# Kernel optimization log

Measured on AMD Instinct MI355X. Metric: run time of the kernel, lower is better.

The kernel has to match this reference:

```python
import jax, jax.numpy as jnp
import numpy as np

LN_EPS = 1e-10


def _log_g(x):
    # log of g(x) where g(x) = x + 0.5 for x >= 0 else sigmoid(x)
    return jnp.where(x >= 0, jnp.log(jax.nn.relu(x) + 0.5), -jax.nn.softplus(-x))


def setup_inputs() -> dict:
    key = jax.random.key(0)
    k1, k2 = jax.random.split(key)
    B, T, D, H = 8, 4096, 512, 512
    x = jax.random.normal(k1, (B, T, D), dtype=jnp.float32)
    ln_gamma = jnp.ones((D,), dtype=jnp.float32)
    ln_beta = jnp.zeros((D,), dtype=jnp.float32)
    W_gh = jax.random.normal(k2, (D, 2 * H), dtype=jnp.float32) * 0.02
    return {"x": x, "ln_gamma": ln_gamma, "ln_beta": ln_beta, "W_gh": W_gh}


def reference(x, ln_gamma, ln_beta, W_gh):
    # LayerNorm over last dim
    mu = jnp.mean(x, axis=-1, keepdims=True)
    var = jnp.mean(jnp.square(x - mu), axis=-1, keepdims=True)
    xn = (x - mu) * jax.lax.rsqrt(var + LN_EPS) * ln_gamma + ln_beta

    # minGRU projection: gate logits k and candidate pre-activation
    gh = jnp.einsum('btd,dh->bth', xn, W_gh)  # [B, T, 2H]
    H = W_gh.shape[1] // 2
    k_gate, h_pre = gh[..., :H], gh[..., H:]

    # log-space parallel scan (Heinsen): h_t = (1-z_t) h_{t-1} + z_t g(h_pre_t)
    log_z = -jax.nn.softplus(-k_gate)        # log sigmoid(k)
    log_coeffs = -jax.nn.softplus(k_gate)    # log(1 - sigmoid(k))
    log_values = log_z + _log_g(h_pre)

    a_star = jnp.cumsum(log_coeffs, axis=1)
    log_h = a_star + jax.lax.cumlogsumexp(log_values - a_star, axis=1)
    h = jnp.exp(log_h)  # [B, T, H]

    # residual (res_proj is Identity since input_size == hidden_size)
    out = h + x
    hidden = h[:, -1]  # last hidden state [B, H]
    return out, hidden
```

## Files before the change

kernel.cpp:

```cpp
#include <hip/hip_runtime.h>
#include <stdint.h>

#define NB 8
#define NT 4096
#define ND 512
#define NH 512
#define NN 1024
#define NM (NB * NT)
#define NK 512
#define NCH 64
#define CTS 64

typedef __bf16 bf16x8 __attribute__((ext_vector_type(8)));
typedef float floatx4 __attribute__((ext_vector_type(4)));
typedef unsigned int uint_g __attribute__((address_space(1)));
typedef unsigned int uint_l __attribute__((address_space(3)));

__device__ __forceinline__ float bf2f(unsigned short u) {
    union { unsigned int i; float f; } v; v.i = ((unsigned int)u) << 16; return v.f;
}
__device__ __forceinline__ unsigned short f2bf(float f) {
    union { float f; unsigned int i; } v; v.f = f;
    return (unsigned short)((v.i + 0x7FFFu + ((v.i >> 16) & 1u)) >> 16);
}

__device__ __forceinline__ void load_lds16(const void* g, void* l) {
    __builtin_amdgcn_global_load_lds((const uint_g*)g, (uint_l*)l, 16, 0, 0);
}

__global__ __launch_bounds__(256) void ln_kernel(const float* __restrict__ x,
                                                 const float* __restrict__ gamma,
                                                 const float* __restrict__ beta,
                                                 unsigned short* __restrict__ xn) {
    int row = blockIdx.x;
    int tid = threadIdx.x;
    float2 v = ((const float2*)(x + (size_t)row * ND))[tid];
    float s  = v.x + v.y;
    float sq = v.x * v.x + v.y * v.y;
#pragma unroll
    for (int off = 32; off > 0; off >>= 1) {
        s  += __shfl_down(s,  off, 64);
        sq += __shfl_down(sq, off, 64);
    }
    __shared__ float ps[4], psq[4];
    __shared__ float smu, srstd;
    int wid = tid >> 6, lane = tid & 63;
    if (lane == 0) { ps[wid] = s; psq[wid] = sq; }
    __syncthreads();
    if (tid == 0) {
        float ts = ps[0] + ps[1] + ps[2] + ps[3];
        float tq = psq[0] + psq[1] + psq[2] + psq[3];
        float mu  = ts * (1.0f / ND);
        float var = tq * (1.0f / ND) - mu * mu;
        smu = mu; srstd = rsqrtf(var + 1e-10f);
    }
    __syncthreads();
    float mu = smu, rstd = srstd;
    float2 g = ((const float2*)gamma)[tid];
    float2 b = ((const float2*)beta)[tid];
    ushort2 o;
    o.x = f2bf((v.x - mu) * rstd * g.x + b.x);
    o.y = f2bf((v.y - mu) * rstd * g.y + b.y);
    ((ushort2*)(xn + (size_t)row * ND))[tid] = o;
}

__global__ __launch_bounds__(256) void wt_kernel(const float* __restrict__ W,
                                                 unsigned short* __restrict__ Wt) {
    __shared__ float tile[32][33];
    int n0 = blockIdx.x * 32;
    int k0 = blockIdx.y * 32;
    int tx = threadIdx.x, ty = threadIdx.y;
#pragma unroll
    for (int j = 0; j < 4; ++j)
        tile[ty + j * 8][tx] = W[(size_t)(k0 + ty + j * 8) * NN + n0 + tx];
    __syncthreads();
#pragma unroll
    for (int j = 0; j < 4; ++j)
        Wt[(size_t)(n0 + ty + j * 8) * NK + k0 + tx] = f2bf(tile[tx][ty + j * 8]);
}

__global__ __launch_bounds__(256) void gemm_kernel(const unsigned short* __restrict__ A,
                                                   const unsigned short* __restrict__ Bt,
                                                   unsigned short* __restrict__ C) {
    __shared__ __align__(16) unsigned short As[128 * 64];
    __shared__ __align__(16) unsigned short Bs[128 * 64];
    int tid  = threadIdx.x;
    int lane = tid & 63;
    int wid  = tid >> 6;
    int wm = wid & 1, wn = wid >> 1;
    int bx = blockIdx.x;
    int mt = bx & 255;
    int nt = bx >> 8;
    const int Rm = mt * 128, Rn = nt * 128;

    int rloc = lane >> 3;
    int cl   = lane & 7;
    int cg   = cl ^ rloc;

    int frow = lane & 15;
    int quad = lane >> 4;
    int fx   = lane & 7;

    floatx4 acc[4][4];
#pragma unroll
    for (int i = 0; i < 4; ++i)
#pragma unroll
        for (int j = 0; j < 4; ++j)
            acc[i][j] = (floatx4){0.f, 0.f, 0.f, 0.f};

#pragma unroll 1
    for (int kt = 0; kt < NK / 64; ++kt) {
        int k0 = kt * 64;
        __syncthreads();
#pragma unroll
        for (int s = 0; s < 4; ++s) {
            int g  = wid * 4 + s;
            int ml = g * 8 + rloc;
            load_lds16(A + (size_t)(Rm + ml) * NK + k0 + cg * 8, As + g * 512);
        }
#pragma unroll
        for (int s = 0; s < 4; ++s) {
            int g  = wid * 4 + s;
            int nl = g * 8 + rloc;
            load_lds16(Bt + (size_t)(Rn + nl) * NK + k0 + cg * 8, Bs + g * 512);
        }
        __syncthreads();
#pragma unroll
        for (int ks = 0; ks < 2; ++ks) {
            int ch = (ks * 4 + quad) ^ fx;
            bf16x8 af[4], bfr[4];
#pragma unroll
            for (int mi = 0; mi < 4; ++mi) {
                int ml = wm * 64 + mi * 16 + frow;
                af[mi] = *(const bf16x8*)(As + ml * 64 + ch * 8);
            }
#pragma unroll
            for (int ni = 0; ni < 4; ++ni) {
                int nl = wn * 64 + ni * 16 + frow;
                bfr[ni] = *(const bf16x8*)(Bs + nl * 64 + ch * 8);
            }
#pragma unroll
            for (int mi = 0; mi < 4; ++mi)
#pragma unroll
                for (int ni = 0; ni < 4; ++ni)
                    acc[mi][ni] = __builtin_amdgcn_mfma_f32_16x16x32_bf16(
                        af[mi], bfr[ni], acc[mi][ni], 0, 0, 0);
        }
    }
#pragma unroll
    for (int mi = 0; mi < 4; ++mi)
#pragma unroll
        for (int ni = 0; ni < 4; ++ni)
#pragma unroll
            for (int r = 0; r < 4; ++r) {
                int row = Rm + wm * 64 + mi * 16 + quad * 4 + r;
                int col = Rn + wn * 64 + ni * 16 + frow;
                C[(size_t)row * NN + col] = f2bf(acc[mi][ni][r]);
            }
}

__device__ __forceinline__ void gate_av(unsigned short ku, unsigned short pu,
                                        float& a, float& v) {
    float k = bf2f(ku), p = bf2f(pu);
    float e = __expf(k);
    a = 1.0f / (1.0f + e);
    float z = e * a;
    float g = (p >= 0.0f) ? (p + 0.5f) : 1.0f / (1.0f + __expf(-p));
    v = z * g;
}

__global__ __launch_bounds__(256) void scan1_kernel(const unsigned short* __restrict__ gh,
                                                    float* __restrict__ cA,
                                                    float* __restrict__ cV) {
    int blk = blockIdx.x;
    int b = blk >> 6, c = blk & 63;
    int h = threadIdx.x * 2;
    const unsigned short* base = gh + ((size_t)(b * NT + c * CTS)) * NN;
    float A0 = 1.f, V0 = 0.f, A1 = 1.f, V1 = 0.f;
#pragma unroll 4
    for (int t = 0; t < CTS; ++t) {
        const unsigned short* p = base + (size_t)t * NN;
        ushort2 kk = *(const ushort2*)(p + h);
        ushort2 hh = *(const ushort2*)(p + NH + h);
        float a0, v0, a1, v1;
        gate_av(kk.x, hh.x, a0, v0);
        gate_av(kk.y, hh.y, a1, v1);
        V0 = a0 * V0 + v0;  A0 *= a0;
        V1 = a1 * V1 + v1;  A1 *= a1;
    }
    size_t o = ((size_t)(b * NCH + c)) * NH + h;
    *(float2*)(cA + o) = make_float2(A0, A1);
    *(float2*)(cV + o) = make_float2(V0, V1);
}

__global__ __launch_bounds__(256) void scan2_kernel(const float* __restrict__ cA,
                                                    const float* __restrict__ cV,
                                                    float* __restrict__ hinit) {
    int w = (blockIdx.x * 256 + threadIdx.x) >> 6;
    int lane = threadIdx.x & 63;
    int b = w >> 9, h = w & 511;
    size_t o = ((size_t)(b * NCH + lane)) * NH + h;
    float A = cA[o], V = cV[o];
#pragma unroll
    for (int off = 1; off < 64; off <<= 1) {
        float Ap = __shfl_up(A, off, 64);
        float Vp = __shfl_up(V, off, 64);
        if (lane >= off) { V = A * Vp + V; A = A * Ap; }
    }
    float Vp = __shfl_up(V, 1, 64);
    hinit[o] = (lane == 0) ? 0.f : Vp;
}

__global__ __launch_bounds__(256) void scan3_kernel(const unsigned short* __restrict__ gh,
                                                    const float* __restrict__ hinit,
                                                    const float* __restrict__ x,
                                                    float* __restrict__ out,
                                                    float* __restrict__ hidden) {
    int blk = blockIdx.x;
    int b = blk >> 6, c = blk & 63;
    int h = threadIdx.x * 2;
    size_t row0 = (size_t)(b * NT + c * CTS);
    const unsigned short* base = gh + row0 * NN;
    const float* xb = x + row0 * ND;
    float* ob = out + row0 * ND;
    float2 hs = *(const float2*)(hinit + ((size_t)(b * NCH + c)) * NH + h);
    float h0 = hs.x, h1 = hs.y;
#pragma unroll 4
    for (int t = 0; t < CTS; ++t) {
        const unsigned short* p = base + (size_t)t * NN;
        ushort2 kk = *(const ushort2*)(p + h);
        ushort2 hh = *(const ushort2*)(p + NH + h);
        float a0, v0, a1, v1;
        gate_av(kk.x, hh.x, a0, v0);
        gate_av(kk.y, hh.y, a1, v1);
        h0 = a0 * h0 + v0;
        h1 = a1 * h1 + v1;
        float2 xv = *(const float2*)(xb + (size_t)t * ND + h);
        *(float2*)(ob + (size_t)t * ND + h) = make_float2(h0 + xv.x, h1 + xv.y);
    }
    if (c == NCH - 1)
        *(float2*)(hidden + (size_t)b * NH + h) = make_float2(h0, h1);
}

extern "C" void kernel_launch(void* const* d_in, const int* in_sizes, int n_in,
                              void* d_out, int out_size, void* d_ws, size_t ws_size,
                              hipStream_t stream) {
    const float* x     = (const float*)d_in[0];
    const float* gamma = (const float*)d_in[1];
    const float* beta  = (const float*)d_in[2];
    const float* W     = (const float*)d_in[3];

    float* out    = (float*)d_out;
    float* hidden = out + (size_t)NM * ND;

    char* ws = (char*)d_ws;
    unsigned short* Wt = (unsigned short*)ws;
    unsigned short* gh = (unsigned short*)(ws + (size_t)(1u << 20));
    float* cA    = (float*)(ws + (size_t)(1u << 20) + (size_t)NM * NN * 2);
    float* cV    = cA + (size_t)NB * NCH * NH;
    float* hinit = cV + (size_t)NB * NCH * NH;
    unsigned short* xn = (unsigned short*)d_out;

    wt_kernel<<<dim3(32, 16), dim3(32, 8), 0, stream>>>(W, Wt);
    ln_kernel<<<NM, 256, 0, stream>>>(x, gamma, beta, xn);
    gemm_kernel<<<2048, 256, 0, stream>>>(xn, Wt, gh);
    scan1_kernel<<<NB * NCH, 256, 0, stream>>>(gh, cA, cV);
    scan2_kernel<<<1024, 256, 0, stream>>>(cA, cV, hinit);
    scan3_kernel<<<NB * NCH, 256, 0, stream>>>(gh, hinit, x, out, hidden);
}
```

Baseline: 260.7 us.

## Rework layernorm per-wave, reorder GEMM tiles, and widen chunked scan kernels

New measurement: 231.8 us. -11.1%, faster.

```diff
diff --git a/kernel.cpp b/kernel.cpp
--- a/kernel.cpp
+++ b/kernel.cpp
@@ -8,8 +8,8 @@
 #define NN 1024
 #define NM (NB * NT)
 #define NK 512
-#define NCH 64
-#define CTS 64
+#define NCH 128
+#define CTS 32
 
 typedef __bf16 bf16x8 __attribute__((ext_vector_type(8)));
 typedef float floatx4 __attribute__((ext_vector_type(4)));
@@ -32,36 +32,38 @@
                                                  const float* __restrict__ gamma,
                                                  const float* __restrict__ beta,
                                                  unsigned short* __restrict__ xn) {
-    int row = blockIdx.x;
-    int tid = threadIdx.x;
-    float2 v = ((const float2*)(x + (size_t)row * ND))[tid];
-    float s  = v.x + v.y;
-    float sq = v.x * v.x + v.y * v.y;
+    int wid = threadIdx.x >> 6, lane = threadIdx.x & 63;
+    size_t row = (size_t)blockIdx.x * 4 + wid;
+    const float4* xr = (const float4*)(x + row * ND);
+    float4 v0 = xr[lane];
+    float4 v1 = xr[lane + 64];
+    float s  = (v0.x + v0.y) + (v0.z + v0.w) + (v1.x + v1.y) + (v1.z + v1.w);
+    float sq = v0.x * v0.x + v0.y * v0.y + v0.z * v0.z + v0.w * v0.w
+             + v1.x * v1.x + v1.y * v1.y + v1.z * v1.z + v1.w * v1.w;
 #pragma unroll
     for (int off = 32; off > 0; off >>= 1) {
-        s  += __shfl_down(s,  off, 64);
-        sq += __shfl_down(sq, off, 64);
-    }
-    __shared__ float ps[4], psq[4];
-    __shared__ float smu, srstd;
-    int wid = tid >> 6, lane = tid & 63;
-    if (lane == 0) { ps[wid] = s; psq[wid] = sq; }
-    __syncthreads();
-    if (tid == 0) {
-        float ts = ps[0] + ps[1] + ps[2] + ps[3];
-        float tq = psq[0] + psq[1] + psq[2] + psq[3];
-        float mu  = ts * (1.0f / ND);
-        float var = tq * (1.0f / ND) - mu * mu;
-        smu = mu; srstd = rsqrtf(var + 1e-10f);
-    }
-    __syncthreads();
-    float mu = smu, rstd = srstd;
-    float2 g = ((const float2*)gamma)[tid];
-    float2 b = ((const float2*)beta)[tid];
-    ushort2 o;
-    o.x = f2bf((v.x - mu) * rstd * g.x + b.x);
-    o.y = f2bf((v.y - mu) * rstd * g.y + b.y);
-    ((ushort2*)(xn + (size_t)row * ND))[tid] = o;
+        s  += __shfl_xor(s,  off, 64);
+        sq += __shfl_xor(sq, off, 64);
+    }
+    float mu   = s * (1.0f / ND);
+    float var  = sq * (1.0f / ND) - mu * mu;
+    float rstd = rsqrtf(var + 1e-10f);
+    const float4* gr = (const float4*)gamma;
+    const float4* br = (const float4*)beta;
+    float4 g0 = gr[lane], g1 = gr[lane + 64];
+    float4 b0 = br[lane], b1 = br[lane + 64];
+    ushort4 o0, o1;
+    o0.x = f2bf((v0.x - mu) * rstd * g0.x + b0.x);
+    o0.y = f2bf((v0.y - mu) * rstd * g0.y + b0.y);
+    o0.z = f2bf((v0.z - mu) * rstd * g0.z + b0.z);
+    o0.w = f2bf((v0.w - mu) * rstd * g0.w + b0.w);
+    o1.x = f2bf((v1.x - mu) * rstd * g1.x + b1.x);
+    o1.y = f2bf((v1.y - mu) * rstd * g1.y + b1.y);
+    o1.z = f2bf((v1.z - mu) * rstd * g1.z + b1.z);
+    o1.w = f2bf((v1.w - mu) * rstd * g1.w + b1.w);
+    ushort4* xo = (ushort4*)(xn + row * ND);
+    xo[lane]      = o0;
+    xo[lane + 64] = o1;
 }
 
 __global__ __launch_bounds__(256) void wt_kernel(const float* __restrict__ W,
@@ -89,8 +91,8 @@
     int wid  = tid >> 6;
     int wm = wid & 1, wn = wid >> 1;
     int bx = blockIdx.x;
-    int mt = bx & 255;
-    int nt = bx >> 8;
+    int nt = bx & 7;
+    int mt = bx >> 3;
     const int Rm = mt * 128, Rn = nt * 128;
 
     int rloc = lane >> 3;
@@ -163,83 +165,93 @@
                                         float& a, float& v) {
     float k = bf2f(ku), p = bf2f(pu);
     float e = __expf(k);
-    a = 1.0f / (1.0f + e);
+    a = __builtin_amdgcn_rcpf(1.0f + e);
     float z = e * a;
-    float g = (p >= 0.0f) ? (p + 0.5f) : 1.0f / (1.0f + __expf(-p));
+    float gneg = __builtin_amdgcn_rcpf(1.0f + __expf(-p));
+    float g = (p >= 0.0f) ? (p + 0.5f) : gneg;
     v = z * g;
 }
 
-__global__ __launch_bounds__(256) void scan1_kernel(const unsigned short* __restrict__ gh,
+__global__ __launch_bounds__(128) void scan1_kernel(const unsigned short* __restrict__ gh,
                                                     float* __restrict__ cA,
                                                     float* __restrict__ cV) {
-    int blk = blockIdx.x;
-    int b = blk >> 6, c = blk & 63;
-    int h = threadIdx.x * 2;
+    int b = blockIdx.x >> 7, c = blockIdx.x & 127;
+    int h = threadIdx.x * 4;
     const unsigned short* base = gh + ((size_t)(b * NT + c * CTS)) * NN;
-    float A0 = 1.f, V0 = 0.f, A1 = 1.f, V1 = 0.f;
-#pragma unroll 4
+    float A0 = 1.f, A1 = 1.f, A2 = 1.f, A3 = 1.f;
+    float V0 = 0.f, V1 = 0.f, V2 = 0.f, V3 = 0.f;
+#pragma unroll 8
     for (int t = 0; t < CTS; ++t) {
         const unsigned short* p = base + (size_t)t * NN;
-        ushort2 kk = *(const ushort2*)(p + h);
-        ushort2 hh = *(const ushort2*)(p + NH + h);
-        float a0, v0, a1, v1;
-        gate_av(kk.x, hh.x, a0, v0);
-        gate_av(kk.y, hh.y, a1, v1);
-        V0 = a0 * V0 + v0;  A0 *= a0;
-        V1 = a1 * V1 + v1;  A1 *= a1;
-    }
-    size_t o = ((size_t)(b * NCH + c)) * NH + h;
-    *(float2*)(cA + o) = make_float2(A0, A1);
-    *(float2*)(cV + o) = make_float2(V0, V1);
+        ushort4 kk = *(const ushort4*)(p + h);
+        ushort4 hh = *(const ushort4*)(p + NH + h);
+        float a, v;
+        gate_av(kk.x, hh.x, a, v); V0 = a * V0 + v; A0 *= a;
+        gate_av(kk.y, hh.y, a, v); V1 = a * V1 + v; A1 *= a;
+        gate_av(kk.z, hh.z, a, v); V2 = a * V2 + v; A2 *= a;
+        gate_av(kk.w, hh.w, a, v); V3 = a * V3 + v; A3 *= a;
+    }
+    size_t o = ((size_t)b * NH + h) * NCH + c;
+    cA[o] = A0; cA[o + NCH] = A1; cA[o + 2 * NCH] = A2; cA[o + 3 * NCH] = A3;
+    cV[o] = V0; cV[o + NCH] = V1; cV[o + 2 * NCH] = V2; cV[o + 3 * NCH] = V3;
 }
 
 __global__ __launch_bounds__(256) void scan2_kernel(const float* __restrict__ cA,
                                                     const float* __restrict__ cV,
                                                     float* __restrict__ hinit) {
-    int w = (blockIdx.x * 256 + threadIdx.x) >> 6;
+    int w = blockIdx.x * 4 + (threadIdx.x >> 6);
     int lane = threadIdx.x & 63;
     int b = w >> 9, h = w & 511;
-    size_t o = ((size_t)(b * NCH + lane)) * NH + h;
-    float A = cA[o], V = cV[o];
+    const float2* a2p = (const float2*)(cA + ((size_t)b * NH + h) * NCH);
+    const float2* v2p = (const float2*)(cV + ((size_t)b * NH + h) * NCH);
+    float2 a2 = a2p[lane];
+    float2 v2 = v2p[lane];
+    float A = a2.y * a2.x;
+    float V = a2.y * v2.x + v2.y;
 #pragma unroll
     for (int off = 1; off < 64; off <<= 1) {
         float Ap = __shfl_up(A, off, 64);
         float Vp = __shfl_up(V, off, 64);
         if (lane >= off) { V = A * Vp + V; A = A * Ap; }
     }
-    float Vp = __shfl_up(V, 1, 64);
-    hinit[o] = (lane == 0) ? 0.f : Vp;
-}
-
-__global__ __launch_bounds__(256) void scan3_kernel(const unsigned short* __restrict__ gh,
+    float excl = __shfl_up(V, 1, 64);
+    if (lane == 0) excl = 0.f;
+    float e0 = excl;
+    float e1 = a2.x * e0 + v2.x;
+    hinit[((size_t)b * NCH + 2 * lane) * NH + h]     = e0;
+    hinit[((size_t)b * NCH + 2 * lane + 1) * NH + h] = e1;
+}
+
+__global__ __launch_bounds__(128) void scan3_kernel(const unsigned short* __restrict__ gh,
                                                     const float* __restrict__ hinit,
                                                     const float* __restrict__ x,
                                                     float* __restrict__ out,
                                                     float* __restrict__ hidden) {
-    int blk = blockIdx.x;
-    int b = blk >> 6, c = blk & 63;
-    int h = threadIdx.x * 2;
+    int b = blockIdx.x >> 7, c = blockIdx.x & 127;
+    int h = threadIdx.x * 4;
     size_t row0 = (size_t)(b * NT + c * CTS);
     const unsigned short* base = gh + row0 * NN;
     const float* xb = x + row0 * ND;
     float* ob = out + row0 * ND;
-    float2 hs = *(const float2*)(hinit + ((size_t)(b * NCH + c)) * NH + h);
-    float h0 = hs.x, h1 = hs.y;
-#pragma unroll 4
+    float4 hv = *(const float4*)(hinit + ((size_t)b * NCH + c) * NH + h);
+#pragma unroll 8
     for (int t = 0; t < CTS; ++t) {
         const unsigned short* p = base + (size_t)t * NN;
-        ushort2 kk = *(const ushort2*)(p + h);
-        ushort2 hh = *(const ushort2*)(p + NH + h);
-        float a0, v0, a1, v1;
-        gate_av(kk.x, hh.x, a0, v0);
-        gate_av(kk.y, hh.y, a1, v1);
-        h0 = a0 * h0 + v0;
-        h1 = a1 * h1 + v1;
-        float2 xv = *(const float2*)(xb + (size_t)t * ND + h);
-        *(float2*)(ob + (size_t)t * ND + h) = make_float2(h0 + xv.x, h1 + xv.y);
+        ushort4 kk = *(const ushort4*)(p + h);
+        ushort4 hh = *(const ushort4*)(p + NH + h);
+        float a, v;
+        gate_av(kk.x, hh.x, a, v); hv.x = a * hv.x + v;
+        gate_av(kk.y, hh.y, a, v); hv.y = a * hv.y + v;
+        gate_av(kk.z, hh.z, a, v); hv.z = a * hv.z + v;
+        gate_av(kk.w, hh.w, a, v); hv.w = a * hv.w + v;
+        float4 xv = *(const float4*)(xb + (size_t)t * ND + h);
+        float4 ov;
+        ov.x = hv.x + xv.x; ov.y = hv.y + xv.y;
+        ov.z = hv.z + xv.z; ov.w = hv.w + xv.w;
+        *(float4*)(ob + (size_t)t * ND + h) = ov;
     }
     if (c == NCH - 1)
-        *(float2*)(hidden + (size_t)b * NH + h) = make_float2(h0, h1);
+        *(float4*)(hidden + (size_t)b * NH + h) = hv;
 }
 
 extern "C" void kernel_launch(void* const* d_in, const int* in_sizes, int n_in,
@@ -262,9 +274,9 @@
     unsigned short* xn = (unsigned short*)d_out;
 
     wt_kernel<<<dim3(32, 16), dim3(32, 8), 0, stream>>>(W, Wt);
-    ln_kernel<<<NM, 256, 0, stream>>>(x, gamma, beta, xn);
+    ln_kernel<<<NM / 4, 256, 0, stream>>>(x, gamma, beta, xn);
     gemm_kernel<<<2048, 256, 0, stream>>>(xn, Wt, gh);
-    scan1_kernel<<<NB * NCH, 256, 0, stream>>>(gh, cA, cV);
+    scan1_kernel<<<NB * NCH, 128, 0, stream>>>(gh, cA, cV);
     scan2_kernel<<<1024, 256, 0, stream>>>(cA, cV, hinit);
-    scan3_kernel<<<NB * NCH, 256, 0, stream>>>(gh, hinit, x, out, hidden);
-}
+    scan3_kernel<<<NB * NCH, 128, 0, stream>>>(gh, hinit, x, out, hidden);
+}
```
